# Kernel tuning notes

Hardware: AMD Instinct MI355X
Metric: run time of the kernel (lower is better)

Reference implementation:

```python
import jax, jax.numpy as jnp
import numpy as np

EPS = 1e-12  # numerical floor for sqrt, stands in for torch pairwise_distance eps


def setup_inputs() -> dict:
    key = jax.random.key(0)
    k1, k2, k3, k4, k5 = jax.random.split(key, 5)
    S, B, E, H, A = 1024, 32, 256, 256, 256
    x = jax.random.normal(k1, (S, B, E), dtype=jnp.float32)
    h = jax.random.normal(k2, (S, B, H), dtype=jnp.float32)
    w_sim = jax.random.normal(k3, (1,), dtype=jnp.float32) * 0.05
    b_sim = jax.random.normal(k4, (1,), dtype=jnp.float32) * 0.05
    W_g = jax.random.normal(k5, (A, 2 * H), dtype=jnp.float32) * 0.05
    b_g = jnp.zeros((A,), dtype=jnp.float32)
    return {"x": x, "h": h, "w_sim": w_sim, "b_sim": b_sim, "W_g": W_g, "b_g": b_g}


def reference(x, h, w_sim, b_sim, W_g, b_g):
    # x: (S,B,E), h: (S,B,H)
    # Pairwise L2 distances per batch element via the gram trick:
    sq = jnp.sum(x * x, axis=-1)                      # (S,B)
    gram = jnp.einsum('tbe,jbe->tbj', x, x)           # (S,B,S)
    d2 = sq[:, :, None] + sq.T[None, :, :] - 2.0 * gram
    dist = jnp.sqrt(jnp.maximum(d2, 0.0) + EPS)       # (S,B,S)
    # weight_sim reduces to scalar affine on the distance (eq. 6 score)
    scores = w_sim[0] * dist + b_sim[0]
    A = jax.nn.softmax(scores, axis=-1)               # softmax over source positions j
    G = jnp.einsum('tbj,jbh->tbh', A, h)              # attention-weighted sum of h
    Z = jnp.tanh(jnp.einsum('tbk,ak->tba', jnp.concatenate([G, h], axis=-1), W_g) + b_g)
    return Z
```

## Files before the change

kernel.cpp:

```cpp
#include <hip/hip_runtime.h>

#define SLEN  1024
#define BATCH 32
#define EDIM  256
#define HDIM  256
#define ADIM  256
#define NTH   256

typedef __attribute__((ext_vector_type(8))) short short8;
typedef __attribute__((ext_vector_type(4))) float f32x4;
typedef __attribute__((ext_vector_type(4))) unsigned int u32x4;

#define XJ_STRIDE 264
#define P_STRIDE  72

#define OFF_XJ  0
#define OFF_HT  33792
#define OFF_P   66560
#define OFF_SQT 75776
#define OFF_SQJ 76032
#define LDS_BYTES 76288

static __device__ __forceinline__ unsigned short f2bf(float f) {
    unsigned int u = __float_as_uint(f);
    u += 0x7FFFu + ((u >> 16) & 1u);
    return (unsigned short)(u >> 16);
}
static __device__ __forceinline__ float bf2f(unsigned short s) {
    return __uint_as_float(((unsigned int)s) << 16);
}

static __device__ __forceinline__ void stage64(const float* __restrict__ src, int row0, int b,
                                               unsigned short* dst, float* sqout, int tid)
{
#pragma unroll
    for (int r = 0; r < 8; ++r) {
        int idx = tid + NTH * r;
        int row = idx >> 5;
        int e8  = idx & 31;
        const float* p = src + ((size_t)(row0 + row) * BATCH + b) * EDIM + e8 * 8;
        float4 v0 = *(const float4*)p;
        float4 v1 = *(const float4*)(p + 4);
        float vv[8] = {v0.x, v0.y, v0.z, v0.w, v1.x, v1.y, v1.z, v1.w};
        short8 pk;
        float s = 0.f;
#pragma unroll
        for (int e = 0; e < 8; ++e) {
            unsigned short us = f2bf(vv[e]);
            pk[e] = (short)us;
            float hf = bf2f(us);
            s += hf * hf;
        }
        *(short8*)(dst + row * XJ_STRIDE + e8 * 8) = pk;
        s += __shfl_xor(s, 1);
        s += __shfl_xor(s, 2);
        s += __shfl_xor(s, 4);
        s += __shfl_xor(s, 8);
        s += __shfl_xor(s, 16);
        if ((tid & 31) == 0) sqout[row] = s;
    }
}

static __device__ __forceinline__ void stage64_split(const float* __restrict__ src, int row0, int b,
                                                     unsigned short* dhi, unsigned short* dlo, int tid)
{
#pragma unroll
    for (int r = 0; r < 8; ++r) {
        int idx = tid + NTH * r;
        int row = idx >> 5;
        int e8  = idx & 31;
        const float* p = src + ((size_t)(row0 + row) * BATCH + b) * HDIM + e8 * 8;
        float4 v0 = *(const float4*)p;
        float4 v1 = *(const float4*)(p + 4);
        float vv[8] = {v0.x, v0.y, v0.z, v0.w, v1.x, v1.y, v1.z, v1.w};
        short8 ph, plo;
#pragma unroll
        for (int e = 0; e < 8; ++e) {
            unsigned short hi = f2bf(vv[e]);
            ph[e] = (short)hi;
            plo[e] = (short)f2bf(vv[e] - bf2f(hi));
        }
        *(short8*)(dhi + row * XJ_STRIDE + e8 * 8) = ph;
        *(short8*)(dlo + row * XJ_STRIDE + e8 * 8) = plo;
    }
}

__global__ __launch_bounds__(NTH, 2)
void fused_mfma(const float* __restrict__ x, const float* __restrict__ h,
                const float* __restrict__ wsim, const float* __restrict__ bsim,
                const float* __restrict__ Wg, const float* __restrict__ bg,
                float* __restrict__ out)
{
    extern __shared__ char smem[];
    unsigned short* xjb    = (unsigned short*)(smem + OFF_XJ);
    char*           htb    = smem + OFF_HT;
    unsigned short* Pl     = (unsigned short*)(smem + OFF_P);
    float*          sqt_l  = (float*)(smem + OFF_SQT);
    float*          sqj_l  = (float*)(smem + OFF_SQJ);
    unsigned short* cat_hi = xjb;
    unsigned short* cat_lo = (unsigned short*)(smem + OFF_HT);

    const int tid  = threadIdx.x;
    const int lane = tid & 63;
    const int w    = tid >> 6;
    const int lr   = lane & 15;
    const int lg   = lane >> 4;

    const int lin = blockIdx.x;
    const int xcd = lin & 7;
    const int kk  = lin >> 3;
    const int b   = (kk >> 4) * 8 + xcd;
    const int t0  = (kk & 15) * 64;

    const float w_s = wsim[0];
    const float b_s = bsim[0];

    stage64(x, t0, b, xjb, sqt_l, tid);
    __syncthreads();
    short8 at[8];
#pragma unroll
    for (int kc = 0; kc < 8; ++kc)
        at[kc] = *(short8*)(xjb + (16 * w + lr) * XJ_STRIDE + kc * 32 + lg * 8);
    float sqt_reg[4];
#pragma unroll
    for (int g2 = 0; g2 < 4; ++g2) sqt_reg[g2] = sqt_l[16 * w + 4 * lg + g2];
    __syncthreads();

    float rsum[4] = {0.f, 0.f, 0.f, 0.f};
    f32x4 Gacc[16];
#pragma unroll
    for (int n = 0; n < 16; ++n) Gacc[n] = (f32x4){0.f, 0.f, 0.f, 0.f};

    const size_t jstride = (size_t)BATCH * HDIM;

    for (int jt = 0; jt < 16; ++jt) {
        const int j0 = jt * 64;
        stage64(x, j0, b, xjb, sqj_l, tid);
        {
            const float* hp = h + (size_t)j0 * jstride + (size_t)b * HDIM + tid;
#pragma unroll
            for (int q = 0; q < 8; ++q) {
                const float* pq = hp + (size_t)(8 * q) * jstride;
                unsigned int d0 = (unsigned int)f2bf(pq[0])           | ((unsigned int)f2bf(pq[jstride]) << 16);
                unsigned int d1 = (unsigned int)f2bf(pq[2 * jstride]) | ((unsigned int)f2bf(pq[3 * jstride]) << 16);
                unsigned int d2 = (unsigned int)f2bf(pq[4 * jstride]) | ((unsigned int)f2bf(pq[5 * jstride]) << 16);
                unsigned int d3 = (unsigned int)f2bf(pq[6 * jstride]) | ((unsigned int)f2bf(pq[7 * jstride]) << 16);
                *(u32x4*)(htb + tid * 128 + 16 * (q ^ (tid & 7))) = (u32x4){d0, d1, d2, d3};
            }
        }
        __syncthreads();

        f32x4 acc[4];
#pragma unroll
        for (int n = 0; n < 4; ++n) {
            acc[n] = (f32x4){0.f, 0.f, 0.f, 0.f};
#pragma unroll
            for (int kc = 0; kc < 8; ++kc) {
                short8 bf = *(short8*)(xjb + (16 * n + lr) * XJ_STRIDE + kc * 32 + lg * 8);
                acc[n] = __builtin_amdgcn_mfma_f32_16x16x32_bf16(at[kc], bf, acc[n], 0, 0, 0);
            }
        }

        float sqjv[4];
#pragma unroll
        for (int n = 0; n < 4; ++n) sqjv[n] = sqj_l[16 * n + lr];
#pragma unroll
        for (int n = 0; n < 4; ++n) {
#pragma unroll
            for (int g2 = 0; g2 < 4; ++g2) {
                float d2v  = sqt_reg[g2] + sqjv[n] - 2.0f * acc[n][g2];
                float dist = sqrtf(fmaxf(d2v, 0.0f) + 1e-12f);
                float pv   = __expf(fmaf(w_s, dist, b_s));
                rsum[g2] += pv;
                Pl[(16 * w + 4 * lg + g2) * P_STRIDE + 16 * n + lr] = f2bf(pv);
            }
        }

        short8 pa0 = *(short8*)(Pl + (16 * w + lr) * P_STRIDE + lg * 8);
        short8 pa1 = *(short8*)(Pl + (16 * w + lr) * P_STRIDE + 32 + lg * 8);
#pragma unroll
        for (int n = 0; n < 16; ++n) {
            int c = 16 * n + lr;
            short8 b0 = *(short8*)(htb + c * 128 + 16 * (lg ^ (c & 7)));
            short8 b1 = *(short8*)(htb + c * 128 + 16 * ((4 + lg) ^ (c & 7)));
            Gacc[n] = __builtin_amdgcn_mfma_f32_16x16x32_bf16(pa0, b0, Gacc[n], 0, 0, 0);
            Gacc[n] = __builtin_amdgcn_mfma_f32_16x16x32_bf16(pa1, b1, Gacc[n], 0, 0, 0);
        }
        __syncthreads();
    }

    float inv[4];
#pragma unroll
    for (int g2 = 0; g2 < 4; ++g2) {
        float s = rsum[g2];
        s += __shfl_xor(s, 1);
        s += __shfl_xor(s, 2);
        s += __shfl_xor(s, 4);
        s += __shfl_xor(s, 8);
        inv[g2] = 1.0f / s;
    }

#pragma unroll
    for (int n = 0; n < 16; ++n) {
#pragma unroll
        for (int g2 = 0; g2 < 4; ++g2) {
            float gn = Gacc[n][g2] * inv[g2];
            unsigned short hi = f2bf(gn);
            unsigned short lo = f2bf(gn - bf2f(hi));
            int t = 16 * w + 4 * lg + g2;
            int c = 16 * n + lr;
            cat_hi[t * XJ_STRIDE + c] = hi;
            cat_lo[t * XJ_STRIDE + c] = lo;
        }
    }
    __syncthreads();

    f32x4 Z[4][4];
#pragma unroll
    for (int m = 0; m < 4; ++m)
#pragma unroll
        for (int n = 0; n < 4; ++n) Z[m][n] = (f32x4){0.f, 0.f, 0.f, 0.f};

    for (int half = 0; half < 2; ++half) {
        if (half == 1) {
            __syncthreads();
            stage64_split(h, t0, b, cat_hi, cat_lo, tid);
            __syncthreads();
        }
#pragma unroll
        for (int kc = 0; kc < 8; ++kc) {
            short8 ah[4], al[4];
#pragma unroll
            for (int m = 0; m < 4; ++m) {
                ah[m] = *(short8*)(cat_hi + (16 * m + lr) * XJ_STRIDE + kc * 32 + lg * 8);
                al[m] = *(short8*)(cat_lo + (16 * m + lr) * XJ_STRIDE + kc * 32 + lg * 8);
            }
#pragma unroll
            for (int n = 0; n < 4; ++n) {
                int a_ = 64 * w + 16 * n + lr;
                const float* wp = Wg + (size_t)a_ * (2 * HDIM) + half * HDIM + kc * 32 + lg * 8;
                float4 wv0 = *(const float4*)wp;
                float4 wv1 = *(const float4*)(wp + 4);
                float vv[8] = {wv0.x, wv0.y, wv0.z, wv0.w, wv1.x, wv1.y, wv1.z, wv1.w};
                short8 bh, bl;
#pragma unroll
                for (int e = 0; e < 8; ++e) {
                    unsigned short hi = f2bf(vv[e]);
                    bh[e] = (short)hi;
                    bl[e] = (short)f2bf(vv[e] - bf2f(hi));
                }
#pragma unroll
                for (int m = 0; m < 4; ++m) {
                    Z[m][n] = __builtin_amdgcn_mfma_f32_16x16x32_bf16(ah[m], bh, Z[m][n], 0, 0, 0);
                    Z[m][n] = __builtin_amdgcn_mfma_f32_16x16x32_bf16(al[m], bh, Z[m][n], 0, 0, 0);
                    Z[m][n] = __builtin_amdgcn_mfma_f32_16x16x32_bf16(ah[m], bl, Z[m][n], 0, 0, 0);
                }
            }
        }
    }

#pragma unroll
    for (int n = 0; n < 4; ++n) {
        int a_ = 64 * w + 16 * n + lr;
        float bgv = bg[a_];
#pragma unroll
        for (int m = 0; m < 4; ++m) {
#pragma unroll
            for (int g2 = 0; g2 < 4; ++g2) {
                int t = 16 * m + 4 * lg + g2;
                float z  = Z[m][n][g2] + bgv;
                float e2 = __expf(2.0f * z);
                float tz = 1.0f - 2.0f / (e2 + 1.0f);
                out[((size_t)(t0 + t) * BATCH + b) * ADIM + a_] = tz;
            }
        }
    }
}

extern "C" void kernel_launch(void* const* d_in, const int* in_sizes, int n_in,
                              void* d_out, int out_size, void* d_ws, size_t ws_size,
                              hipStream_t stream) {
    const float* x    = (const float*)d_in[0];
    const float* h    = (const float*)d_in[1];
    const float* wsim = (const float*)d_in[2];
    const float* bsim = (const float*)d_in[3];
    const float* Wg   = (const float*)d_in[4];
    const float* bg   = (const float*)d_in[5];
    float* out = (float*)d_out;

    (void)hipFuncSetAttribute((const void*)fused_mfma,
                              hipFuncAttributeMaxDynamicSharedMemorySize, LDS_BYTES);
    hipLaunchKernelGGL(fused_mfma, dim3(512), dim3(NTH), LDS_BYTES, stream,
                       x, h, wsim, bsim, Wg, bg, out);
}
```

Measured before the change: 275.6 us.

## Precompute bf16 swizzled operands in workspace and stream them via global_load_lds

Adds preprocessing kernels that convert x, h and W_g to bf16 (with hi/lo splits for h and W_g), write them in batch-major swizzled layouts, precompute squared norms, and build a transposed h. A new fused kernel then loads these tiles straight into LDS with global_load_lds instead of converting fp32 inside the main loop for every t-tile. The aim is to remove the conversion and norm work that each block repeated and to shrink main-loop traffic. The cost is three extra launches, about 64MB of workspace reads and writes, and a fallback to the old kernel when the workspace is too small.

```diff
diff --git a/kernel.cpp b/kernel.cpp
--- a/kernel.cpp
+++ b/kernel.cpp
@@ -10,10 +10,319 @@
 typedef __attribute__((ext_vector_type(8))) short short8;
 typedef __attribute__((ext_vector_type(4))) float f32x4;
 typedef __attribute__((ext_vector_type(4))) unsigned int u32x4;
+typedef __attribute__((ext_vector_type(4))) unsigned short ushort4v;
+
+#define XBF_OFF  0u
+#define HT_OFF   16777216u
+#define HHI_OFF  33554432u
+#define HLO_OFF  50331648u
+#define WGHI_OFF 67108864u
+#define WGLO_OFF 67371008u
+#define SQX_OFF  67633152u
+#define WS_NEED  67764224u
+
+static __device__ __forceinline__ unsigned short f2bf(float f) {
+    unsigned int u = __float_as_uint(f);
+    u += 0x7FFFu + ((u >> 16) & 1u);
+    return (unsigned short)(u >> 16);
+}
+static __device__ __forceinline__ float bf2f(unsigned short s) {
+    return __uint_as_float(((unsigned int)s) << 16);
+}
+static __device__ __forceinline__ void gload16(const void* g, void* l) {
+    __builtin_amdgcn_global_load_lds(
+        (const __attribute__((address_space(1))) unsigned int*)g,
+        (__attribute__((address_space(3))) unsigned int*)l, 16, 0, 0);
+}
+
+__global__ __launch_bounds__(NTH)
+void pre_convert(const float* __restrict__ x, const float* __restrict__ h,
+                 unsigned short* __restrict__ xbf, unsigned short* __restrict__ hhi,
+                 unsigned short* __restrict__ hlo, float* __restrict__ sqx)
+{
+    const int blk = blockIdx.x, tid = threadIdx.x;
+    const int isx = (blk < 4096);
+    const int rblk = isx ? blk : blk - 4096;
+    const int row = rblk * 8 + (tid >> 5);
+    const int j = row >> 5, b = row & 31;
+    const int chunk = tid & 31;
+    const float* p = (isx ? x : h) + (size_t)row * 256 + chunk * 8;
+    float4 v0 = *(const float4*)p, v1 = *(const float4*)(p + 4);
+    float vv[8] = {v0.x, v0.y, v0.z, v0.w, v1.x, v1.y, v1.z, v1.w};
+    short8 hi8;
+    float lof[8];
+    float s = 0.f;
+#pragma unroll
+    for (int e = 0; e < 8; ++e) {
+        unsigned short us = f2bf(vv[e]);
+        hi8[e] = (short)us;
+        float hf = bf2f(us);
+        s += hf * hf;
+        lof[e] = vv[e] - hf;
+    }
+    const size_t dst = ((size_t)b * 1024 + j) * 256 + (size_t)((chunk ^ (j & 7)) * 8);
+    if (isx) {
+        *(short8*)(xbf + dst) = hi8;
+        s += __shfl_xor(s, 1);
+        s += __shfl_xor(s, 2);
+        s += __shfl_xor(s, 4);
+        s += __shfl_xor(s, 8);
+        s += __shfl_xor(s, 16);
+        if ((tid & 31) == 0) sqx[b * 1024 + j] = s;
+    } else {
+        *(short8*)(hhi + dst) = hi8;
+        short8 lo8;
+#pragma unroll
+        for (int e = 0; e < 8; ++e) lo8[e] = (short)f2bf(lof[e]);
+        *(short8*)(hlo + dst) = lo8;
+    }
+}
+
+__global__ __launch_bounds__(NTH)
+void pre_ht(const float* __restrict__ h, unsigned short* __restrict__ hT)
+{
+    __shared__ unsigned short tl[64][72];
+    const int blk = blockIdx.x, tid = threadIdx.x;
+    const int b = blk & 31, jt = (blk >> 5) & 15, ct = blk >> 9;
+    const int jj0 = tid >> 4, cq = tid & 15;
+#pragma unroll
+    for (int it = 0; it < 4; ++it) {
+        int jj = jj0 + it * 16;
+        const float* p = h + ((size_t)(jt * 64 + jj) * BATCH + b) * HDIM + ct * 64 + cq * 4;
+        float4 v = *(const float4*)p;
+        ushort4v u;
+        u.x = f2bf(v.x); u.y = f2bf(v.y); u.z = f2bf(v.z); u.w = f2bf(v.w);
+        *(ushort4v*)&tl[jj][cq * 4] = u;
+    }
+    __syncthreads();
+#pragma unroll
+    for (int it = 0; it < 2; ++it) {
+        int idx = tid + it * 256;
+        int cc = idx >> 3, slot = idx & 7;
+        int chunk = slot ^ (cc & 7);
+        short8 o;
+#pragma unroll
+        for (int e = 0; e < 8; ++e) o[e] = (short)tl[chunk * 8 + e][cc];
+        *(short8*)(hT + ((size_t)b * 256 + ct * 64 + cc) * 1024 + jt * 64 + slot * 8) = o;
+    }
+}
+
+__global__ __launch_bounds__(NTH)
+void pre_wg(const float* __restrict__ Wg, unsigned short* __restrict__ wghi,
+            unsigned short* __restrict__ wglo)
+{
+    const int id = blockIdx.x * NTH + threadIdx.x;
+    const float* p = Wg + (size_t)id * 8;
+    float4 v0 = *(const float4*)p, v1 = *(const float4*)(p + 4);
+    float vv[8] = {v0.x, v0.y, v0.z, v0.w, v1.x, v1.y, v1.z, v1.w};
+    short8 hi8, lo8;
+#pragma unroll
+    for (int e = 0; e < 8; ++e) {
+        unsigned short hi = f2bf(vv[e]);
+        hi8[e] = (short)hi;
+        lo8[e] = (short)f2bf(vv[e] - bf2f(hi));
+    }
+    *(short8*)(wghi + (size_t)id * 8) = hi8;
+    *(short8*)(wglo + (size_t)id * 8) = lo8;
+}
+
+#define L_XJ 0
+#define L_HT 32768
+#define L_P  65536
+#define LDS2_BYTES 74752
+
+__global__ __launch_bounds__(NTH, 2)
+void fused2(const unsigned short* __restrict__ xbf, const unsigned short* __restrict__ hT,
+            const unsigned short* __restrict__ hhi, const unsigned short* __restrict__ hlo,
+            const unsigned short* __restrict__ wghi, const unsigned short* __restrict__ wglo,
+            const float* __restrict__ sqx, const float* __restrict__ wsim,
+            const float* __restrict__ bsim, const float* __restrict__ bg,
+            float* __restrict__ out)
+{
+    extern __shared__ char smem[];
+    char* XJ = smem + L_XJ;
+    char* HT = smem + L_HT;
+    unsigned short* Pl = (unsigned short*)(smem + L_P);
+
+    const int tid  = threadIdx.x;
+    const int lane = tid & 63;
+    const int w    = tid >> 6;
+    const int lr   = lane & 15;
+    const int lg   = lane >> 4;
+    const int key  = lr & 7;
+
+    const int lin = blockIdx.x;
+    const int xcd = lin & 7;
+    const int kk  = lin >> 3;
+    const int b   = (kk >> 4) * 8 + xcd;
+    const int t0  = (kk & 15) * 64;
+
+    const float w_s = wsim[0];
+    const float b_s = bsim[0];
+
+    short8 at[8];
+    {
+        const unsigned short* rp = xbf + ((size_t)b * 1024 + t0 + 16 * w + lr) * 256;
+#pragma unroll
+        for (int kc = 0; kc < 8; ++kc)
+            at[kc] = *(const short8*)(rp + (((kc * 4 + lg) ^ key) << 3));
+    }
+    float sqt_reg[4];
+#pragma unroll
+    for (int g2 = 0; g2 < 4; ++g2) sqt_reg[g2] = sqx[b * 1024 + t0 + 16 * w + 4 * lg + g2];
+
+    float rsum[4] = {0.f, 0.f, 0.f, 0.f};
+    f32x4 Gacc[16];
+#pragma unroll
+    for (int n = 0; n < 16; ++n) Gacc[n] = (f32x4){0.f, 0.f, 0.f, 0.f};
+
+    for (int jt = 0; jt < 16; ++jt) {
+        const int j0 = jt * 64;
+        {
+            const char* sx = (const char*)(xbf + ((size_t)b * 1024 + j0 + 16 * w) * 256);
+            char* dx = XJ + 16 * w * 512;
+#pragma unroll
+            for (int i = 0; i < 8; ++i)
+                gload16(sx + i * 1024 + lane * 16, dx + i * 1024);
+        }
+        {
+#pragma unroll
+            for (int i = 0; i < 8; ++i) {
+                const char* sh = (const char*)(hT + ((size_t)b * 256 + 64 * w + i * 8 + (lane >> 3)) * 1024)
+                                 + jt * 128 + (lane & 7) * 16;
+                gload16(sh, HT + w * 8192 + i * 1024);
+            }
+        }
+        float sqjv[4];
+#pragma unroll
+        for (int n = 0; n < 4; ++n) sqjv[n] = sqx[b * 1024 + j0 + 16 * n + lr];
+        __syncthreads();
+
+        f32x4 acc[4];
+#pragma unroll
+        for (int n = 0; n < 4; ++n) {
+            acc[n] = (f32x4){0.f, 0.f, 0.f, 0.f};
+#pragma unroll
+            for (int kc = 0; kc < 8; ++kc) {
+                short8 bf = *(const short8*)(XJ + (16 * n + lr) * 512 + (((kc * 4 + lg) ^ key) << 4));
+                acc[n] = __builtin_amdgcn_mfma_f32_16x16x32_bf16(at[kc], bf, acc[n], 0, 0, 0);
+            }
+        }
+
+#pragma unroll
+        for (int n = 0; n < 4; ++n) {
+#pragma unroll
+            for (int g2 = 0; g2 < 4; ++g2) {
+                float d2v  = sqt_reg[g2] + sqjv[n] - 2.0f * acc[n][g2];
+                float dist = sqrtf(fmaxf(d2v, 0.0f) + 1e-12f);
+                float pv   = __expf(fmaf(w_s, dist, b_s));
+                rsum[g2] += pv;
+                Pl[(16 * w + 4 * lg + g2) * 72 + 16 * n + lr] = f2bf(pv);
+            }
+        }
+
+        short8 pa0 = *(const short8*)(Pl + (16 * w + lr) * 72 + lg * 8);
+        short8 pa1 = *(const short8*)(Pl + (16 * w + lr) * 72 + 32 + lg * 8);
+#pragma unroll
+        for (int n = 0; n < 16; ++n) {
+            const char* hrow = HT + (16 * n + lr) * 128;
+            short8 b0 = *(const short8*)(hrow + ((lg ^ key) << 4));
+            short8 b1 = *(const short8*)(hrow + (((4 + lg) ^ key) << 4));
+            Gacc[n] = __builtin_amdgcn_mfma_f32_16x16x32_bf16(pa0, b0, Gacc[n], 0, 0, 0);
+            Gacc[n] = __builtin_amdgcn_mfma_f32_16x16x32_bf16(pa1, b1, Gacc[n], 0, 0, 0);
+        }
+        __syncthreads();
+    }
+
+    float inv[4];
+#pragma unroll
+    for (int g2 = 0; g2 < 4; ++g2) {
+        float s = rsum[g2];
+        s += __shfl_xor(s, 1);
+        s += __shfl_xor(s, 2);
+        s += __shfl_xor(s, 4);
+        s += __shfl_xor(s, 8);
+        inv[g2] = 1.0f / s;
+    }
+
+#pragma unroll
+    for (int n = 0; n < 16; ++n) {
+#pragma unroll
+        for (int g2 = 0; g2 < 4; ++g2) {
+            int t = 16 * w + 4 * lg + g2;
+            int c = 16 * n + lr;
+            float gn = Gacc[n][g2] * inv[g2];
+            unsigned short hi = f2bf(gn);
+            unsigned short lo = f2bf(gn - bf2f(hi));
+            int off = t * 512 + (((c >> 3) ^ (t & 7)) << 4) + ((c & 7) << 1);
+            *(unsigned short*)(XJ + off) = hi;
+            *(unsigned short*)(HT + off) = lo;
+        }
+    }
+    __syncthreads();
+
+    f32x4 Z[4][4];
+#pragma unroll
+    for (int m = 0; m < 4; ++m)
+#pragma unroll
+        for (int n = 0; n < 4; ++n) Z[m][n] = (f32x4){0.f, 0.f, 0.f, 0.f};
+
+    for (int half = 0; half < 2; ++half) {
+        if (half == 1) {
+            __syncthreads();
+            const char* shi = (const char*)(hhi + ((size_t)b * 1024 + t0 + 16 * w) * 256);
+            const char* slo = (const char*)(hlo + ((size_t)b * 1024 + t0 + 16 * w) * 256);
+#pragma unroll
+            for (int i = 0; i < 8; ++i)
+                gload16(shi + i * 1024 + lane * 16, XJ + 16 * w * 512 + i * 1024);
+#pragma unroll
+            for (int i = 0; i < 8; ++i)
+                gload16(slo + i * 1024 + lane * 16, HT + 16 * w * 512 + i * 1024);
+            __syncthreads();
+        }
+#pragma unroll
+        for (int kc = 0; kc < 8; ++kc) {
+            short8 ah[4], al[4];
+#pragma unroll
+            for (int m = 0; m < 4; ++m) {
+                int off = (16 * m + lr) * 512 + (((kc * 4 + lg) ^ key) << 4);
+                ah[m] = *(const short8*)(XJ + off);
+                al[m] = *(const short8*)(HT + off);
+            }
+#pragma unroll
+            for (int n = 0; n < 4; ++n) {
+                int a_ = 64 * w + 16 * n + lr;
+                short8 bh = *(const short8*)(wghi + (size_t)a_ * 512 + half * 256 + kc * 32 + lg * 8);
+                short8 bl = *(const short8*)(wglo + (size_t)a_ * 512 + half * 256 + kc * 32 + lg * 8);
+#pragma unroll
+                for (int m = 0; m < 4; ++m) {
+                    Z[m][n] = __builtin_amdgcn_mfma_f32_16x16x32_bf16(ah[m], bh, Z[m][n], 0, 0, 0);
+                    Z[m][n] = __builtin_amdgcn_mfma_f32_16x16x32_bf16(al[m], bh, Z[m][n], 0, 0, 0);
+                    Z[m][n] = __builtin_amdgcn_mfma_f32_16x16x32_bf16(ah[m], bl, Z[m][n], 0, 0, 0);
+                }
+            }
+        }
+    }
+
+#pragma unroll
+    for (int n = 0; n < 4; ++n) {
+        int a_ = 64 * w + 16 * n + lr;
+        float bgv = bg[a_];
+#pragma unroll
+        for (int m = 0; m < 4; ++m) {
+#pragma unroll
+            for (int g2 = 0; g2 < 4; ++g2) {
+                int t = 16 * m + 4 * lg + g2;
+                float z  = Z[m][n][g2] + bgv;
+                float e2 = __expf(2.0f * z);
+                out[((size_t)(t0 + t) * BATCH + b) * ADIM + a_] = 1.0f - 2.0f / (e2 + 1.0f);
+            }
+        }
+    }
+}
 
 #define XJ_STRIDE 264
 #define P_STRIDE  72
-
 #define OFF_XJ  0
 #define OFF_HT  33792
 #define OFF_P   66560
@@ -21,23 +330,13 @@
 #define OFF_SQJ 76032
 #define LDS_BYTES 76288
 
-static __device__ __forceinline__ unsigned short f2bf(float f) {
-    unsigned int u = __float_as_uint(f);
-    u += 0x7FFFu + ((u >> 16) & 1u);
-    return (unsigned short)(u >> 16);
-}
-static __device__ __forceinline__ float bf2f(unsigned short s) {
-    return __uint_as_float(((unsigned int)s) << 16);
-}
-
 static __device__ __forceinline__ void stage64(const float* __restrict__ src, int row0, int b,
                                                unsigned short* dst, float* sqout, int tid)
 {
 #pragma unroll
     for (int r = 0; r < 8; ++r) {
         int idx = tid + NTH * r;
-        int row = idx >> 5;
-        int e8  = idx & 31;
+        int row = idx >> 5, e8 = idx & 31;
         const float* p = src + ((size_t)(row0 + row) * BATCH + b) * EDIM + e8 * 8;
         float4 v0 = *(const float4*)p;
         float4 v1 = *(const float4*)(p + 4);
@@ -67,8 +366,7 @@
 #pragma unroll
     for (int r = 0; r < 8; ++r) {
         int idx = tid + NTH * r;
-        int row = idx >> 5;
-        int e8  = idx & 31;
+        int row = idx >> 5, e8 = idx & 31;
         const float* p = src + ((size_t)(row0 + row) * BATCH + b) * HDIM + e8 * 8;
         float4 v0 = *(const float4*)p;
         float4 v1 = *(const float4*)(p + 4);
@@ -270,8 +568,7 @@
                 int t = 16 * m + 4 * lg + g2;
                 float z  = Z[m][n][g2] + bgv;
                 float e2 = __expf(2.0f * z);
-                float tz = 1.0f - 2.0f / (e2 + 1.0f);
-                out[((size_t)(t0 + t) * BATCH + b) * ADIM + a_] = tz;
+                out[((size_t)(t0 + t) * BATCH + b) * ADIM + a_] = 1.0f - 2.0f / (e2 + 1.0f);
             }
         }
     }
@@ -288,8 +585,28 @@
     const float* bg   = (const float*)d_in[5];
     float* out = (float*)d_out;
 
-    (void)hipFuncSetAttribute((const void*)fused_mfma,
-                              hipFuncAttributeMaxDynamicSharedMemorySize, LDS_BYTES);
-    hipLaunchKernelGGL(fused_mfma, dim3(512), dim3(NTH), LDS_BYTES, stream,
-                       x, h, wsim, bsim, Wg, bg, out);
-}
+    if (ws_size >= (size_t)WS_NEED && d_ws != nullptr) {
+        char* ws = (char*)d_ws;
+        unsigned short* xbf  = (unsigned short*)(ws + XBF_OFF);
+        unsigned short* hTg  = (unsigned short*)(ws + HT_OFF);
+        unsigned short* hhi  = (unsigned short*)(ws + HHI_OFF);
+        unsigned short* hlo  = (unsigned short*)(ws + HLO_OFF);
+        unsigned short* wghi = (unsigned short*)(ws + WGHI_OFF);
+        unsigned short* wglo = (unsigned short*)(ws + WGLO_OFF);
+        float*          sqx  = (float*)(ws + SQX_OFF);
+
+        hipLaunchKernelGGL(pre_convert, dim3(8192), dim3(NTH), 0, stream, x, h, xbf, hhi, hlo, sqx);
+        hipLaunchKernelGGL(pre_ht,      dim3(2048), dim3(NTH), 0, stream, h, hTg);
+        hipLaunchKernelGGL(pre_wg,      dim3(64),   dim3(NTH), 0, stream, Wg, wghi, wglo);
+
+        (void)hipFuncSetAttribute((const void*)fused2,
+                                  hipFuncAttributeMaxDynamicSharedMemorySize, LDS2_BYTES);
+        hipLaunchKernelGGL(fused2, dim3(512), dim3(NTH), LDS2_BYTES, stream,
+                           xbf, hTg, hhi, hlo, wghi, wglo, sqx, wsim, bsim, bg, out);
+    } else {
+        (void)hipFuncSetAttribute((const void*)fused_mfma,
+                                  hipFuncAttributeMaxDynamicSharedMemorySize, LDS_BYTES);
+        hipLaunchKernelGGL(fused_mfma, dim3(512), dim3(NTH), LDS_BYTES, stream,
+                           x, h, wsim, bsim, Wg, bg, out);
+    }
+}
```

New measurement: 226.7 us. 1.22x faster.
